# Kernel optimization log

Measured on AMD Instinct MI355X. Metric: run time of the kernel, lower is better.

## Reference

```python
import jax, jax.numpy as jnp
import numpy as np

N, V, D, F, E, H = 10000, 4, 3, 128, 320000, 128
EDGE_IN = 2 * F + 2 * V  # node_features[senders] + node_features[receivers] + lengths_x^2 + lengths_y^2
NORM_CONST = 1.0


def setup_inputs() -> dict:
    key = jax.random.key(0)
    ks = jax.random.split(key, 20)
    w = lambda k, shape: jax.random.normal(k, shape, jnp.float32) * 0.05
    z = lambda n: jnp.zeros((n,), jnp.float32)
    return dict(
        node_positions=jax.random.normal(ks[0], (N, V, D), jnp.float32),
        node_vectors=jax.random.normal(ks[1], (N, V, D), jnp.float32),
        node_features=jax.random.normal(ks[2], (N, F), jnp.float32),
        senders=jax.random.randint(ks[3], (E,), 0, N),
        receivers=jax.random.randint(ks[4], (E,), 0, N),
        We0=w(ks[5], (EDGE_IN, H)), be0=z(H), We1=w(ks[6], (H, H)), be1=z(H),
        Winf=w(ks[7], (H, 1)), binf=z(1),
        Wx0=w(ks[8], (H, H)), bx0=z(H), Wx1=w(ks[9], (H, H)), bx1=z(H), Wxf=w(ks[10], (H, V)),
        Wy0=w(ks[11], (H, H)), by0=z(H), Wy1=w(ks[12], (H, H)), by1=z(H), Wyf=w(ks[13], (H, V)),
        Wh0=w(ks[14], (H + F, H)), bh0=z(H), Wh1=w(ks[15], (H, H)), bh1=z(H), Wh2=w(ks[16], (H, F)), bh2=z(F),
    )


def reference(node_positions, node_vectors, node_features, senders, receivers,
              We0, be0, We1, be1, Winf, binf,
              Wx0, bx0, Wx1, bx1, Wxf,
              Wy0, by0, Wy1, by1, Wyf,
              Wh0, bh0, Wh1, bh1, Wh2, bh2):
    act = jax.nn.silu
    n_nodes = node_positions.shape[0]
    avg = int(np.sqrt(receivers.shape[0]))  # avg_num_neighbours as in source

    def radial(coord):  # coord: [N, V, D]
        d = coord[receivers] - coord[senders]              # [E, V, D]
        l = jnp.sqrt(jnp.sum(d * d, axis=-1) + 1e-8)       # [E, V] safe_norm
        d = d / (NORM_CONST + l[:, :, None])               # normalize=True
        return l, d

    lx, dx = radial(node_positions)
    ly, dy = radial(node_vectors)

    ef = jnp.concatenate([node_features[senders], node_features[receivers],
                          lx ** 2, ly ** 2], axis=-1)      # [E, 264]
    m = act(act(ef @ We0 + be0) @ We1 + be1)               # phi_e, activate_final=True

    # phi_x: torso MLP + no-bias head, tanh
    px = jnp.tanh(act(act(m @ Wx0 + bx0) @ Wx1 + bx1) @ Wxf)          # [E, V]
    shifts_x = jax.ops.segment_sum(dx * px[:, :, None], receivers, num_segments=n_nodes) / avg

    # phi_y: torso MLP + no-bias head, tanh
    py = jnp.tanh(act(act(m @ Wy0 + by0) @ Wy1 + by1) @ Wyf)          # [E, V]
    shifts_y = jax.ops.segment_sum(dy * py[:, :, None], receivers, num_segments=n_nodes) / avg

    # attention gate on messages
    m = m * jax.nn.sigmoid(m @ Winf + binf)
    m_i = jax.ops.segment_sum(m, receivers, num_segments=n_nodes) / avg

    # phi_h (activate_final=False) + residual_h
    hin = jnp.concatenate([m_i, node_features], axis=-1)
    features_out = act(act(hin @ Wh0 + bh0) @ Wh1 + bh1) @ Wh2 + bh2 + node_features

    skip = shifts_y
    vectors_out = skip + node_vectors            # residual_y
    positions_out = shifts_x + node_positions    # x_update='x', residual_x
    return positions_out, vectors_out, features_out, skip
```

## Files before the change

kernel.cpp:

```cpp
#include <hip/hip_runtime.h>
#include <math.h>

#define NN 10000
#define EE 320000
#define TE 32
#define TN 16
#define INV_AVG (1.0f / 565.0f)

#define OUT_POS 0
#define OUT_VEC 120000
#define OUT_FEAT 240000
#define OUT_SKIP 1520000
#define OUT_TOTAL 1640000

#define WS_WE0 0
#define WS_WE1 36864
#define WS_WX0 53248
#define WS_WX1 69632
#define WS_WY0 86016
#define WS_WY1 102400
#define WS_WH0 118784
#define WS_WH1 151552
#define WS_WH2 167936
#define WS_WXF 184320
#define WS_WYF 186368
#define WS_OFF_NF 376832
#define WS_OFF_SORT 2936832
#define WS_OFF_CNT  4216832
#define WS_OFF_CUR  4256832

typedef __attribute__((ext_vector_type(8))) short bfrag;
typedef __attribute__((ext_vector_type(4))) float f4acc;

__device__ __forceinline__ float siluf(float x) {
    return x * __builtin_amdgcn_rcpf(1.0f + __expf(-x));
}
__device__ __forceinline__ float tanh_fast(float x) {
    return 1.0f - 2.0f * __builtin_amdgcn_rcpf(__expf(2.0f * x) + 1.0f);
}
__device__ __forceinline__ float sigmoid_fast(float x) {
    return __builtin_amdgcn_rcpf(1.0f + __expf(-x));
}
__device__ __forceinline__ unsigned int cvt_pk_bf16(float lo, float hi) {
    unsigned int r;
    asm("v_cvt_pk_bf16_f32 %0, %1, %2" : "=v"(r) : "v"(lo), "v"(hi));
    return r;
}
__device__ __forceinline__ unsigned short f2bf(float x) {
    union { float f; unsigned int u; } c; c.f = x;
    unsigned int r = c.u + 0x7FFFu + ((c.u >> 16) & 1u);
    return (unsigned short)(r >> 16);
}
__device__ __forceinline__ float bf2f(unsigned short h) {
    union { unsigned int u; float f; } c; c.u = ((unsigned int)h) << 16; return c.f;
}

__global__ __launch_bounds__(256) void init_kernel(const float* __restrict__ pos,
                                                   float* __restrict__ out,
                                                   int* __restrict__ cnt)
{
    int idx = blockIdx.x * 256 + threadIdx.x;
    if (idx < OUT_TOTAL) out[idx] = (idx < 120000) ? pos[idx] : 0.0f;
    if (idx < NN) cnt[idx] = 0;
}

__global__ __launch_bounds__(256) void prep_all(
    const float* __restrict__ nf, unsigned short* __restrict__ nfb,
    const int* __restrict__ rcv, int* __restrict__ cnt,
    const float* __restrict__ We0, const float* __restrict__ be0,
    const float* __restrict__ We1,
    const float* __restrict__ Wx0, const float* __restrict__ Wx1,
    const float* __restrict__ Wy0, const float* __restrict__ Wy1,
    const float* __restrict__ Wh0, const float* __restrict__ Wh1,
    const float* __restrict__ Wh2,
    const float* __restrict__ Wxf, const float* __restrict__ Wyf,
    unsigned short* __restrict__ wsW)
{
    int tid = blockIdx.x * 256 + threadIdx.x;
    int i = tid * 8;
    if (i < NN * 128) {
        float4 a = *(const float4*)(nf + i);
        float4 b = *(const float4*)(nf + i + 4);
        uint4 pk;
        pk.x = cvt_pk_bf16(a.x, a.y);
        pk.y = cvt_pk_bf16(a.z, a.w);
        pk.z = cvt_pk_bf16(b.x, b.y);
        pk.w = cvt_pk_bf16(b.z, b.w);
        *(uint4*)(nfb + i) = pk;
    }
    int e = tid * 2;
    if (e < EE) {
        atomicAdd(cnt + rcv[e], 1);
        atomicAdd(cnt + rcv[e + 1], 1);
    }
    if (tid >= 23552) return;
    if (tid >= 23040) {
        const float* Wf = (tid < 23296) ? Wxf : Wyf;
        unsigned short* dst = wsW + ((tid < 23296) ? WS_WXF : WS_WYF);
        int rel = tid - ((tid < 23296) ? 23040 : 23296);
        int kc = rel >> 6, lane = rel & 63;
        int lhi = lane >> 4, llo = lane & 15;
        unsigned short* o = dst + ((kc * 64 + lane) << 3);
#pragma unroll
        for (int j = 0; j < 8; ++j) {
            int k = kc * 32 + lhi * 8 + j;
            o[j] = (llo < 4) ? f2bf(Wf[k * 4 + llo]) : (unsigned short)0;
        }
        return;
    }
    const float* W; unsigned short* dst; int Kact = 128, rel; int isWe0 = 0;
    if (tid < 4608)        { W = We0; dst = wsW + WS_WE0; Kact = 264; rel = tid; isWe0 = 1; }
    else if (tid < 14848)  {
        int r = tid - 4608; int m = r >> 11; rel = r & 2047;
        switch (m) {
            case 0: W = We1; dst = wsW + WS_WE1; break;
            case 1: W = Wx0; dst = wsW + WS_WX0; break;
            case 2: W = Wx1; dst = wsW + WS_WX1; break;
            case 3: W = Wy0; dst = wsW + WS_WY0; break;
            default: W = Wy1; dst = wsW + WS_WY1; break;
        }
    }
    else if (tid < 18944)  { W = Wh0; dst = wsW + WS_WH0; Kact = 256; rel = tid - 14848; }
    else if (tid < 20992)  { W = Wh1; dst = wsW + WS_WH1; rel = tid - 18944; }
    else                   { W = Wh2; dst = wsW + WS_WH2; rel = tid - 20992; }
    int lane = rel & 63, oc = (rel >> 6) & 7, kc = rel >> 9;
    int k0 = kc * 32 + ((lane >> 4) << 3);
    int col = oc * 16 + (lane & 15);
    unsigned short* o = dst + (((kc * 8 + oc) * 64 + lane) << 3);
#pragma unroll
    for (int j = 0; j < 8; ++j) {
        int k = k0 + j;
        unsigned short v = 0;
        if (k < Kact) v = f2bf(W[k * 128 + col]);
        else if (isWe0 && k == 264) v = f2bf(be0[col]);
        o[j] = v;
    }
}

__global__ __launch_bounds__(1024) void scan_kernel(const int* __restrict__ cnt,
                                                    int* __restrict__ cursor)
{
    __shared__ int wsum[16];
    int t = threadIdx.x;
    int lane = t & 63, wid = t >> 6;
    int base = t * 10;
    int c[10];
    int s = 0;
#pragma unroll
    for (int i = 0; i < 10; ++i) {
        int b = base + i;
        c[i] = (b < NN) ? cnt[b] : 0;
        s += c[i];
    }
    int run = s;
#pragma unroll
    for (int off = 1; off < 64; off <<= 1) {
        int v = __shfl_up(run, off);
        if (lane >= off) run += v;
    }
    if (lane == 63) wsum[wid] = run;
    __syncthreads();
    if (t < 16) {
        int v = wsum[t];
#pragma unroll
        for (int off = 1; off < 16; off <<= 1) {
            int u = __shfl_up(v, off);
            if (t >= off) v += u;
        }
        wsum[t] = v;
    }
    __syncthreads();
    int wave_excl = (wid == 0) ? 0 : wsum[wid - 1];
    int excl = wave_excl + run - s;
#pragma unroll
    for (int i = 0; i < 10; ++i) {
        int b = base + i;
        if (b < NN) { cursor[b] = excl; excl += c[i]; }
    }
}

__global__ __launch_bounds__(256) void scatter_sort_kernel(const int* __restrict__ rcv,
                                                           int* __restrict__ cursor,
                                                           int* __restrict__ sortedIdx)
{
    int e = blockIdx.x * 256 + threadIdx.x;
    if (e < EE) {
        int slot = atomicAdd(cursor + rcv[e], 1);
        sortedIdx[slot] = e;
    }
}

template<int KC, int MT, int NT>
__device__ __forceinline__ void gemm_lds(const unsigned short* __restrict__ fragW,
                                         const unsigned short* Bld, const int bstride,
                                         const int tile0, const int lane,
                                         f4acc acc[MT][NT])
{
    const int lhi = lane >> 4, llo = lane & 15;
#pragma unroll
    for (int kc = 0; kc < KC; ++kc) {
        bfrag b[NT];
#pragma unroll
        for (int nt = 0; nt < NT; ++nt)
            b[nt] = *(const bfrag*)(Bld + (nt * 16 + llo) * bstride + kc * 32 + lhi * 8);
#pragma unroll
        for (int i = 0; i < MT; ++i) {
            bfrag a = *(const bfrag*)(fragW + (((kc * 8 + tile0 + i) * 64 + lane) << 3));
#pragma unroll
            for (int nt = 0; nt < NT; ++nt)
                acc[i][nt] = __builtin_amdgcn_mfma_f32_16x16x32_bf16(a, b[nt], acc[i][nt], 0, 0, 0);
        }
    }
}

template<int NT>
__device__ __forceinline__ void epilogue_silu_t(f4acc acc[2][NT], const float* __restrict__ bias,
                                                unsigned short* Dld, int lane, int w)
{
    const int lhi = lane >> 4, llo = lane & 15;
#pragma unroll
    for (int i = 0; i < 2; ++i) {
        int ch = (w * 2 + i) * 16 + lhi * 4;
        float4 bv = *(const float4*)(bias + ch);
#pragma unroll
        for (int nt = 0; nt < NT; ++nt) {
            uint2 pk;
            pk.x = cvt_pk_bf16(siluf(acc[i][nt][0] + bv.x), siluf(acc[i][nt][1] + bv.y));
            pk.y = cvt_pk_bf16(siluf(acc[i][nt][2] + bv.z), siluf(acc[i][nt][3] + bv.w));
            *(uint2*)(Dld + (nt * 16 + llo) * 136 + ch) = pk;
        }
    }
}

__device__ __forceinline__ void epilogue_silu_nobias(f4acc acc[2][2],
                                                     unsigned short* Dld, int lane, int w)
{
    const int lhi = lane >> 4, llo = lane & 15;
#pragma unroll
    for (int i = 0; i < 2; ++i) {
        int ch = (w * 2 + i) * 16 + lhi * 4;
#pragma unroll
        for (int nt = 0; nt < 2; ++nt) {
            uint2 pk;
            pk.x = cvt_pk_bf16(siluf(acc[i][nt][0]), siluf(acc[i][nt][1]));
            pk.y = cvt_pk_bf16(siluf(acc[i][nt][2]), siluf(acc[i][nt][3]));
            *(uint2*)(Dld + (nt * 16 + llo) * 136 + ch) = pk;
        }
    }
}

__global__ __launch_bounds__(256, 6) void edge_kernel(
    const float* __restrict__ pos, const float* __restrict__ vec,
    const unsigned short* __restrict__ nfb,
    const int* __restrict__ snd, const int* __restrict__ rcv,
    const int* __restrict__ sortedIdx,
    const unsigned short* __restrict__ wsW,
    const float* __restrict__ be1,
    const float* __restrict__ Winf, const float* __restrict__ binf,
    const float* __restrict__ bx0, const float* __restrict__ bx1,
    const float* __restrict__ by0, const float* __restrict__ by1,
    float* outPos, float* outSkip, float* outFeat)
{
    __shared__ unsigned short L2T[TE * 40];
    __shared__ unsigned short H0[TE * 136];
    __shared__ unsigned short Hm[TE * 136];
    __shared__ float dstore[TE * 24];
    __shared__ float pxy[TE * 8];
    __shared__ float gateacc[TE];
    __shared__ int sidx[TE], ridx[TE];

    const int t = threadIdx.x;
    const int lane = t & 63, w = t >> 6;
    const int lhi = lane >> 4, llo = lane & 15;
    const int e_base = blockIdx.x * TE;

    if (t < TE) {
        int eid = sortedIdx[e_base + t];
        int sn = snd[eid], rn = rcv[eid];
        sidx[t] = sn; ridx[t] = rn;
#pragma unroll
        for (int tensor = 0; tensor < 2; ++tensor) {
            const float* c = tensor ? vec : pos;
#pragma unroll
            for (int v = 0; v < 4; ++v) {
                float d0 = c[rn * 12 + v * 3 + 0] - c[sn * 12 + v * 3 + 0];
                float d1 = c[rn * 12 + v * 3 + 1] - c[sn * 12 + v * 3 + 1];
                float d2 = c[rn * 12 + v * 3 + 2] - c[sn * 12 + v * 3 + 2];
                float ss = fmaf(d0, d0, fmaf(d1, d1, d2 * d2)) + 1e-8f;
                float l = sqrtf(ss);
                float inv = __builtin_amdgcn_rcpf(1.0f + l);
                L2T[t * 40 + tensor * 4 + v] = f2bf(ss);
                dstore[t * 24 + tensor * 12 + v * 3 + 0] = d0 * inv;
                dstore[t * 24 + tensor * 12 + v * 3 + 1] = d1 * inv;
                dstore[t * 24 + tensor * 12 + v * 3 + 2] = d2 * inv;
            }
        }
#pragma unroll
        for (int j = 0; j < 6; ++j)
            *(uint2*)(L2T + t * 40 + 8 + j * 4) = make_uint2(0u, 0u);
        L2T[t * 40 + 8] = 0x3F80u;
    }
    if (t >= 64 && t < 96) gateacc[t - 64] = 0.0f;
    __syncthreads();

    {
        const int sn0 = sidx[llo], sn1 = sidx[16 + llo];
        const int rn0 = ridx[llo], rn1 = ridx[16 + llo];
        const unsigned short* s0 = nfb + sn0 * 128 + lhi * 8;
        const unsigned short* s1 = nfb + sn1 * 128 + lhi * 8;
        const unsigned short* r0 = nfb + rn0 * 128 + lhi * 8;
        const unsigned short* r1 = nfb + rn1 * 128 + lhi * 8;
        const int mt0 = w * 2;
        f4acc acc[2][2];
#pragma unroll
        for (int i = 0; i < 2; ++i) { acc[i][0] = (f4acc){0.f,0.f,0.f,0.f}; acc[i][1] = (f4acc){0.f,0.f,0.f,0.f}; }
#pragma unroll
        for (int kc = 0; kc < 8; ++kc) {
            bfrag b0 = *(const bfrag*)((kc < 4 ? s0 : r0) + (kc & 3) * 32);
            bfrag b1 = *(const bfrag*)((kc < 4 ? s1 : r1) + (kc & 3) * 32);
#pragma unroll
            for (int i = 0; i < 2; ++i) {
                bfrag a = *(const bfrag*)(wsW + WS_WE0 + (((kc * 8 + mt0 + i) * 64 + lane) << 3));
                acc[i][0] = __builtin_amdgcn_mfma_f32_16x16x32_bf16(a, b0, acc[i][0], 0, 0, 0);
                acc[i][1] = __builtin_amdgcn_mfma_f32_16x16x32_bf16(a, b1, acc[i][1], 0, 0, 0);
            }
        }
        {
            bfrag b0 = *(const bfrag*)(L2T + llo * 40 + lhi * 8);
            bfrag b1 = *(const bfrag*)(L2T + (16 + llo) * 40 + lhi * 8);
#pragma unroll
            for (int i = 0; i < 2; ++i) {
                bfrag a = *(const bfrag*)(wsW + WS_WE0 + (((8 * 8 + mt0 + i) * 64 + lane) << 3));
                acc[i][0] = __builtin_amdgcn_mfma_f32_16x16x32_bf16(a, b0, acc[i][0], 0, 0, 0);
                acc[i][1] = __builtin_amdgcn_mfma_f32_16x16x32_bf16(a, b1, acc[i][1], 0, 0, 0);
            }
        }
        epilogue_silu_nobias(acc, H0, lane, w);
    }
    __syncthreads();

    {
        f4acc acc[2][2];
#pragma unroll
        for (int i = 0; i < 2; ++i) { acc[i][0] = (f4acc){0.f,0.f,0.f,0.f}; acc[i][1] = (f4acc){0.f,0.f,0.f,0.f}; }
        gemm_lds<4, 2, 2>(wsW + WS_WE1, H0, 136, w * 2, lane, acc);
        float gp0 = 0.0f, gp1 = 0.0f;
#pragma unroll
        for (int i = 0; i < 2; ++i) {
            int ch = (w * 2 + i) * 16 + lhi * 4;
            float4 bv = *(const float4*)(be1 + ch);
            float4 wg = *(const float4*)(Winf + ch);
#pragma unroll
            for (int nt = 0; nt < 2; ++nt) {
                float v0 = siluf(acc[i][nt][0] + bv.x);
                float v1 = siluf(acc[i][nt][1] + bv.y);
                float v2 = siluf(acc[i][nt][2] + bv.z);
                float v3 = siluf(acc[i][nt][3] + bv.w);
                uint2 pk;
                pk.x = cvt_pk_bf16(v0, v1);
                pk.y = cvt_pk_bf16(v2, v3);
                *(uint2*)(Hm + (nt * 16 + llo) * 136 + ch) = pk;
                float g = fmaf(v0, wg.x, fmaf(v1, wg.y, fmaf(v2, wg.z, v3 * wg.w)));
                if (nt == 0) gp0 += g; else gp1 += g;
            }
        }
        gp0 += __shfl_xor(gp0, 16); gp0 += __shfl_xor(gp0, 32);
        gp1 += __shfl_xor(gp1, 16); gp1 += __shfl_xor(gp1, 32);
        if (lane < 16) {
            atomicAdd(&gateacc[lane], gp0);
            atomicAdd(&gateacc[16 + lane], gp1);
        }
    }
    __syncthreads();

#pragma unroll 1
    for (int br = 0; br < 2; ++br) {
        {
            const unsigned short* fw = wsW + (br ? WS_WY0 : WS_WX0);
            const float* bias = br ? by0 : bx0;
            f4acc acc[2][2];
#pragma unroll
            for (int i = 0; i < 2; ++i) { acc[i][0] = (f4acc){0.f,0.f,0.f,0.f}; acc[i][1] = (f4acc){0.f,0.f,0.f,0.f}; }
            gemm_lds<4, 2, 2>(fw, Hm, 136, w * 2, lane, acc);
            epilogue_silu_t<2>(acc, bias, H0, lane, w);
        }
        __syncthreads();
        {
            const unsigned short* fw = wsW + (br ? WS_WY1 : WS_WX1);
            const float* bias = br ? by1 : bx1;
            f4acc acc[2][2];
#pragma unroll
            for (int i = 0; i < 2; ++i) { acc[i][0] = (f4acc){0.f,0.f,0.f,0.f}; acc[i][1] = (f4acc){0.f,0.f,0.f,0.f}; }
            gemm_lds<4, 2, 2>(fw, H0, 136, w * 2, lane, acc);
            __syncthreads();
            epilogue_silu_t<2>(acc, bias, H0, lane, w);
        }
        __syncthreads();
        if (w < 2) {
            const unsigned short* fw = wsW + (br ? WS_WYF : WS_WXF);
            f4acc h = (f4acc){0.f, 0.f, 0.f, 0.f};
#pragma unroll
            for (int kc = 0; kc < 4; ++kc) {
                bfrag b = *(const bfrag*)(H0 + (w * 16 + llo) * 136 + kc * 32 + lhi * 8);
                bfrag a = *(const bfrag*)(fw + ((kc * 64 + lane) << 3));
                h = __builtin_amdgcn_mfma_f32_16x16x32_bf16(a, b, h, 0, 0, 0);
            }
            if (lhi == 0) {
#pragma unroll
                for (int v = 0; v < 4; ++v)
                    pxy[(w * 16 + llo) * 8 + br * 4 + v] = h[v];
            }
        }
        __syncthreads();
    }

    pxy[t] = tanh_fast(pxy[t]) * INV_AVG;
    if (t < TE) gateacc[t] = sigmoid_fast(gateacc[t] + binf[0]) * INV_AVG;
    __syncthreads();

    if (t < 128) {
        int half = t >> 6, pair = t & 63;
        int jj = pair * 2;
        int e0h = half * 16;
        float a0 = 0.0f, a1 = 0.0f;
        int prev_r = ridx[e0h];
#pragma unroll
        for (int i = 0; i < 16; ++i) {
            int e = e0h + i;
            int r = ridx[e];
            if (r != prev_r) {
                atomicAdd(outFeat + prev_r * 128 + jj, a0);
                atomicAdd(outFeat + prev_r * 128 + jj + 1, a1);
                a0 = a1 = 0.0f;
                prev_r = r;
            }
            unsigned int pk = *(const unsigned int*)(Hm + e * 136 + jj);
            float g = gateacc[e];
            a0 = fmaf(bf2f((unsigned short)(pk & 0xffffu)), g, a0);
            a1 = fmaf(bf2f((unsigned short)(pk >> 16)), g, a1);
        }
        atomicAdd(outFeat + prev_r * 128 + jj, a0);
        atomicAdd(outFeat + prev_r * 128 + jj + 1, a1);
    } else if (t >= 208) {
        int s = t - 208;
        int c = s >> 1, half = s & 1;
        int tensor = (c >= 12) ? 1 : 0;
        int rem = c - tensor * 12;
        int v = rem / 3;
        float* dstp = tensor ? outSkip : outPos;
        int e0h = half * 16;
        float acc = 0.0f;
        int prev_r = ridx[e0h];
#pragma unroll
        for (int i = 0; i < 16; ++i) {
            int e = e0h + i;
            int r = ridx[e];
            if (r != prev_r) {
                atomicAdd(dstp + prev_r * 12 + rem, acc);
                acc = 0.0f;
                prev_r = r;
            }
            acc = fmaf(dstore[e * 24 + c], pxy[e * 8 + tensor * 4 + v], acc);
        }
        atomicAdd(dstp + prev_r * 12 + rem, acc);
    }
}

__global__ __launch_bounds__(256) void node_kernel(
    const float* __restrict__ nf, const unsigned short* __restrict__ nfb,
    const float* __restrict__ nvec,
    const unsigned short* __restrict__ wsW,
    const float* __restrict__ bh0, const float* __restrict__ bh1,
    const float* __restrict__ bh2,
    float* outFeat , float* outVec,
    const float* __restrict__ outSkip)
{
    __shared__ unsigned short A[TN * 264];
    __shared__ unsigned short H1[TN * 136];
    __shared__ unsigned short H2b[TN * 136];
    const int t = threadIdx.x;
    const int lane = t & 63, w = t >> 6;
    const int lhi = lane >> 4, llo = lane & 15;
    const int n_base = blockIdx.x * TN;

#pragma unroll
    for (int it = 0; it < 4; ++it) {
        int idx = t + it * 256;
        int row = idx >> 6, q = idx & 63;
        int n = n_base + row;
        float2 v = make_float2(0.f, 0.f);
        if (n < NN) v = *(const float2*)(outFeat + n * 128 + q * 2);
        *(unsigned int*)(A + row * 264 + q * 2) = cvt_pk_bf16(v.x, v.y);
    }
    {
        int row = t >> 4, q = t & 15;
        int n = n_base + row;
        uint4 v = make_uint4(0u, 0u, 0u, 0u);
        if (n < NN) v = *(const uint4*)(nfb + n * 128 + q * 8);
        *(uint4*)(A + row * 264 + 128 + q * 8) = v;
    }
    __syncthreads();
    {
        f4acc acc[2][1];
        acc[0][0] = (f4acc){0.f,0.f,0.f,0.f}; acc[1][0] = (f4acc){0.f,0.f,0.f,0.f};
        gemm_lds<8, 2, 1>(wsW + WS_WH0, A, 264, w * 2, lane, acc);
        epilogue_silu_t<1>(acc, bh0, H1, lane, w);
    }
    __syncthreads();
    {
        f4acc acc[2][1];
        acc[0][0] = (f4acc){0.f,0.f,0.f,0.f}; acc[1][0] = (f4acc){0.f,0.f,0.f,0.f};
        gemm_lds<4, 2, 1>(wsW + WS_WH1, H1, 136, w * 2, lane, acc);
        epilogue_silu_t<1>(acc, bh1, H2b, lane, w);
    }
    __syncthreads();
    {
        f4acc acc[2][1];
        acc[0][0] = (f4acc){0.f,0.f,0.f,0.f}; acc[1][0] = (f4acc){0.f,0.f,0.f,0.f};
        gemm_lds<4, 2, 1>(wsW + WS_WH2, H2b, 136, w * 2, lane, acc);
#pragma unroll
        for (int i = 0; i < 2; ++i) {
            int ch = (w * 2 + i) * 16 + lhi * 4;
            float4 bv = *(const float4*)(bh2 + ch);
            int n = n_base + llo;
            if (n < NN) {
                float4 r = *(const float4*)(nf + n * 128 + ch);
                float4 o;
                o.x = acc[i][0][0] + bv.x + r.x;
                o.y = acc[i][0][1] + bv.y + r.y;
                o.z = acc[i][0][2] + bv.z + r.z;
                o.w = acc[i][0][3] + bv.w + r.w;
                *(float4*)(outFeat + n * 128 + ch) = o;
            }
        }
    }
    if (t < TN * 12) {
        int n = n_base + t / 12;
        if (n < NN) {
            int g = n_base * 12 + t;
            outVec[g] = outSkip[g] + nvec[g];
        }
    }
}

extern "C" void kernel_launch(void* const* d_in, const int* in_sizes, int n_in,
                              void* d_out, int out_size, void* d_ws, size_t ws_size,
                              hipStream_t stream)
{
    (void)in_sizes; (void)n_in; (void)out_size; (void)ws_size;

    const float* pos  = (const float*)d_in[0];
    const float* vecv = (const float*)d_in[1];
    const float* nf   = (const float*)d_in[2];
    const int*   snd  = (const int*)d_in[3];
    const int*   rcv  = (const int*)d_in[4];
    const float* We0  = (const float*)d_in[5];
    const float* be0  = (const float*)d_in[6];
    const float* We1  = (const float*)d_in[7];
    const float* be1  = (const float*)d_in[8];
    const float* Winf = (const float*)d_in[9];
    const float* binf = (const float*)d_in[10];
    const float* Wx0  = (const float*)d_in[11];
    const float* bx0  = (const float*)d_in[12];
    const float* Wx1  = (const float*)d_in[13];
    const float* bx1  = (const float*)d_in[14];
    const float* Wxf  = (const float*)d_in[15];
    const float* Wy0  = (const float*)d_in[16];
    const float* by0  = (const float*)d_in[17];
    const float* Wy1  = (const float*)d_in[18];
    const float* by1  = (const float*)d_in[19];
    const float* Wyf  = (const float*)d_in[20];
    const float* Wh0  = (const float*)d_in[21];
    const float* bh0  = (const float*)d_in[22];
    const float* Wh1  = (const float*)d_in[23];
    const float* bh1  = (const float*)d_in[24];
    const float* Wh2  = (const float*)d_in[25];
    const float* bh2  = (const float*)d_in[26];

    float* out     = (float*)d_out;
    float* outPos  = out + OUT_POS;
    float* outVec  = out + OUT_VEC;
    float* outFeat = out + OUT_FEAT;
    float* outSkip = out + OUT_SKIP;

    char* ws = (char*)d_ws;
    unsigned short* wsW = (unsigned short*)ws;
    unsigned short* nfb = (unsigned short*)(ws + WS_OFF_NF);
    int* sortedIdx      = (int*)(ws + WS_OFF_SORT);
    int* cnt            = (int*)(ws + WS_OFF_CNT);
    int* cursor         = (int*)(ws + WS_OFF_CUR);

    init_kernel<<<(OUT_TOTAL + 255) / 256, 256, 0, stream>>>(pos, out, cnt);

    prep_all<<<(NN * 128 / 8 + 255) / 256, 256, 0, stream>>>(
        nf, nfb, rcv, cnt,
        We0, be0, We1, Wx0, Wx1, Wy0, Wy1, Wh0, Wh1, Wh2, Wxf, Wyf, wsW);

    scan_kernel<<<1, 1024, 0, stream>>>(cnt, cursor);
    scatter_sort_kernel<<<(EE + 255) / 256, 256, 0, stream>>>(rcv, cursor, sortedIdx);

    edge_kernel<<<EE / TE, 256, 0, stream>>>(
        pos, vecv, nfb, snd, rcv, sortedIdx, wsW,
        be1, Winf, binf,
        bx0, bx1, by0, by1,
        outPos, outSkip, outFeat);

    node_kernel<<<(NN + TN - 1) / TN, 256, 0, stream>>>(
        nf, nfb, vecv, wsW, bh0, bh1, bh2,
        outFeat, outVec, outSkip);
}
```

Baseline: 234.3 us.

## Make edge kernel wave-independent with per-wave 16-edge tiles, no block barriers

```diff
diff --git a/kernel.cpp b/kernel.cpp
--- a/kernel.cpp
+++ b/kernel.cpp
@@ -3,7 +3,6 @@
 
 #define NN 10000
 #define EE 320000
-#define TE 32
 #define TN 16
 #define INV_AVG (1.0f / 565.0f)
 
@@ -32,6 +31,8 @@
 typedef __attribute__((ext_vector_type(8))) short bfrag;
 typedef __attribute__((ext_vector_type(4))) float f4acc;
 
+#define FENCE() asm volatile("s_waitcnt lgkmcnt(0)" ::: "memory")
+
 __device__ __forceinline__ float siluf(float x) {
     return x * __builtin_amdgcn_rcpf(1.0f + __expf(-x));
 }
@@ -190,66 +191,44 @@
     }
 }
 
-template<int KC, int MT, int NT>
-__device__ __forceinline__ void gemm_lds(const unsigned short* __restrict__ fragW,
-                                         const unsigned short* Bld, const int bstride,
-                                         const int tile0, const int lane,
-                                         f4acc acc[MT][NT])
+template<int KC>
+__device__ __forceinline__ void gemm_w(const unsigned short* __restrict__ fragW,
+                                       const unsigned short* Bld, int lane,
+                                       f4acc acc[8])
 {
     const int lhi = lane >> 4, llo = lane & 15;
 #pragma unroll
     for (int kc = 0; kc < KC; ++kc) {
-        bfrag b[NT];
-#pragma unroll
-        for (int nt = 0; nt < NT; ++nt)
-            b[nt] = *(const bfrag*)(Bld + (nt * 16 + llo) * bstride + kc * 32 + lhi * 8);
-#pragma unroll
-        for (int i = 0; i < MT; ++i) {
-            bfrag a = *(const bfrag*)(fragW + (((kc * 8 + tile0 + i) * 64 + lane) << 3));
-#pragma unroll
-            for (int nt = 0; nt < NT; ++nt)
-                acc[i][nt] = __builtin_amdgcn_mfma_f32_16x16x32_bf16(a, b[nt], acc[i][nt], 0, 0, 0);
-        }
-    }
-}
-
-template<int NT>
-__device__ __forceinline__ void epilogue_silu_t(f4acc acc[2][NT], const float* __restrict__ bias,
-                                                unsigned short* Dld, int lane, int w)
+        bfrag b = *(const bfrag*)(Bld + llo * 136 + kc * 32 + lhi * 8);
+#pragma unroll
+        for (int mt = 0; mt < 8; ++mt) {
+            bfrag a = *(const bfrag*)(fragW + (((kc * 8 + mt) * 64 + lane) << 3));
+            acc[mt] = __builtin_amdgcn_mfma_f32_16x16x32_bf16(a, b, acc[mt], 0, 0, 0);
+        }
+    }
+}
+
+template<bool HASBIAS>
+__device__ __forceinline__ void epi_w(f4acc acc[8], const float* __restrict__ bias,
+                                      unsigned short* Dld, int lane)
 {
     const int lhi = lane >> 4, llo = lane & 15;
 #pragma unroll
-    for (int i = 0; i < 2; ++i) {
-        int ch = (w * 2 + i) * 16 + lhi * 4;
-        float4 bv = *(const float4*)(bias + ch);
-#pragma unroll
-        for (int nt = 0; nt < NT; ++nt) {
-            uint2 pk;
-            pk.x = cvt_pk_bf16(siluf(acc[i][nt][0] + bv.x), siluf(acc[i][nt][1] + bv.y));
-            pk.y = cvt_pk_bf16(siluf(acc[i][nt][2] + bv.z), siluf(acc[i][nt][3] + bv.w));
-            *(uint2*)(Dld + (nt * 16 + llo) * 136 + ch) = pk;
-        }
-    }
-}
-
-__device__ __forceinline__ void epilogue_silu_nobias(f4acc acc[2][2],
-                                                     unsigned short* Dld, int lane, int w)
-{
-    const int lhi = lane >> 4, llo = lane & 15;
-#pragma unroll
-    for (int i = 0; i < 2; ++i) {
-        int ch = (w * 2 + i) * 16 + lhi * 4;
-#pragma unroll
-        for (int nt = 0; nt < 2; ++nt) {
-            uint2 pk;
-            pk.x = cvt_pk_bf16(siluf(acc[i][nt][0]), siluf(acc[i][nt][1]));
-            pk.y = cvt_pk_bf16(siluf(acc[i][nt][2]), siluf(acc[i][nt][3]));
-            *(uint2*)(Dld + (nt * 16 + llo) * 136 + ch) = pk;
-        }
-    }
-}
-
-__global__ __launch_bounds__(256, 6) void edge_kernel(
+    for (int mt = 0; mt < 8; ++mt) {
+        int ch = mt * 16 + lhi * 4;
+        float bx = 0.f, by = 0.f, bz = 0.f, bw = 0.f;
+        if (HASBIAS) {
+            float4 bv = *(const float4*)(bias + ch);
+            bx = bv.x; by = bv.y; bz = bv.z; bw = bv.w;
+        }
+        uint2 pk;
+        pk.x = cvt_pk_bf16(siluf(acc[mt][0] + bx), siluf(acc[mt][1] + by));
+        pk.y = cvt_pk_bf16(siluf(acc[mt][2] + bz), siluf(acc[mt][3] + bw));
+        *(uint2*)(Dld + llo * 136 + ch) = pk;
+    }
+}
+
+__global__ __launch_bounds__(256, 3) void edge_kernel(
     const float* __restrict__ pos, const float* __restrict__ vec,
     const unsigned short* __restrict__ nfb,
     const int* __restrict__ snd, const int* __restrict__ rcv,
@@ -261,208 +240,234 @@
     const float* __restrict__ by0, const float* __restrict__ by1,
     float* outPos, float* outSkip, float* outFeat)
 {
-    __shared__ unsigned short L2T[TE * 40];
-    __shared__ unsigned short H0[TE * 136];
-    __shared__ unsigned short Hm[TE * 136];
-    __shared__ float dstore[TE * 24];
-    __shared__ float pxy[TE * 8];
-    __shared__ float gateacc[TE];
-    __shared__ int sidx[TE], ridx[TE];
+    __shared__ __align__(16) unsigned short HwS[4][16 * 136];
+    __shared__ __align__(16) unsigned short MwS[4][16 * 136];
+    __shared__ __align__(16) unsigned short L2TS[4][16 * 40];
+    __shared__ float dstoreS[4][16 * 24];
+    __shared__ float pxyS[4][16 * 8];
+    __shared__ float gatevS[4][16];
+    __shared__ int sidxS[4][16], ridxS[4][16];
 
     const int t = threadIdx.x;
     const int lane = t & 63, w = t >> 6;
     const int lhi = lane >> 4, llo = lane & 15;
-    const int e_base = blockIdx.x * TE;
-
-    if (t < TE) {
-        int eid = sortedIdx[e_base + t];
-        int sn = snd[eid], rn = rcv[eid];
-        sidx[t] = sn; ridx[t] = rn;
-#pragma unroll
-        for (int tensor = 0; tensor < 2; ++tensor) {
-            const float* c = tensor ? vec : pos;
-#pragma unroll
-            for (int v = 0; v < 4; ++v) {
-                float d0 = c[rn * 12 + v * 3 + 0] - c[sn * 12 + v * 3 + 0];
-                float d1 = c[rn * 12 + v * 3 + 1] - c[sn * 12 + v * 3 + 1];
-                float d2 = c[rn * 12 + v * 3 + 2] - c[sn * 12 + v * 3 + 2];
-                float ss = fmaf(d0, d0, fmaf(d1, d1, d2 * d2)) + 1e-8f;
-                float l = sqrtf(ss);
-                float inv = __builtin_amdgcn_rcpf(1.0f + l);
-                L2T[t * 40 + tensor * 4 + v] = f2bf(ss);
-                dstore[t * 24 + tensor * 12 + v * 3 + 0] = d0 * inv;
-                dstore[t * 24 + tensor * 12 + v * 3 + 1] = d1 * inv;
-                dstore[t * 24 + tensor * 12 + v * 3 + 2] = d2 * inv;
+
+    unsigned short* Hw = HwS[w];
+    unsigned short* Mw = MwS[w];
+    unsigned short* L2T = L2TS[w];
+    float* dstore = dstoreS[w];
+    float* pxy = pxyS[w];
+    float* gatev = gatevS[w];
+    int* sidx = sidxS[w];
+    int* ridx = ridxS[w];
+
+    const int e_base = blockIdx.x * 64 + w * 16;
+
+    if (lane < 16) {
+        int eid = sortedIdx[e_base + lane];
+        sidx[lane] = snd[eid];
+        ridx[lane] = rcv[eid];
+    }
+    if (lane < 48) {
+        int e = lane / 3, q = lane - (lane / 3) * 3;
+        uint4 z = make_uint4(q == 0 ? 0x3F80u : 0u, 0u, 0u, 0u);
+        *(uint4*)(L2T + e * 40 + 8 + q * 8) = z;
+    }
+    FENCE();
+#pragma unroll
+    for (int it = 0; it < 2; ++it) {
+        int task = lane + it * 64;
+        int e = task >> 3, sub = task & 7;
+        int tensor = sub >> 2, v = sub & 3;
+        const float* c = tensor ? vec : pos;
+        int sn = sidx[e], rn = ridx[e];
+        float d0 = c[rn * 12 + v * 3 + 0] - c[sn * 12 + v * 3 + 0];
+        float d1 = c[rn * 12 + v * 3 + 1] - c[sn * 12 + v * 3 + 1];
+        float d2 = c[rn * 12 + v * 3 + 2] - c[sn * 12 + v * 3 + 2];
+        float ss = fmaf(d0, d0, fmaf(d1, d1, d2 * d2)) + 1e-8f;
+        float l = sqrtf(ss);
+        float inv = __builtin_amdgcn_rcpf(1.0f + l);
+        L2T[e * 40 + tensor * 4 + v] = f2bf(ss);
+        dstore[e * 24 + tensor * 12 + v * 3 + 0] = d0 * inv;
+        dstore[e * 24 + tensor * 12 + v * 3 + 1] = d1 * inv;
+        dstore[e * 24 + tensor * 12 + v * 3 + 2] = d2 * inv;
+    }
+    FENCE();
+
+    f4acc acc[8];
+#pragma unroll
+    for (int mt = 0; mt < 8; ++mt) acc[mt] = (f4acc){0.f, 0.f, 0.f, 0.f};
+    {
+        const unsigned short* s = nfb + sidx[llo] * 128 + lhi * 8;
+        const unsigned short* r = nfb + ridx[llo] * 128 + lhi * 8;
+#pragma unroll
+        for (int kc = 0; kc < 8; ++kc) {
+            bfrag b = *(const bfrag*)((kc < 4 ? s : r) + (kc & 3) * 32);
+#pragma unroll
+            for (int mt = 0; mt < 8; ++mt) {
+                bfrag a = *(const bfrag*)(wsW + WS_WE0 + (((kc * 8 + mt) * 64 + lane) << 3));
+                acc[mt] = __builtin_amdgcn_mfma_f32_16x16x32_bf16(a, b, acc[mt], 0, 0, 0);
             }
         }
-#pragma unroll
-        for (int j = 0; j < 6; ++j)
-            *(uint2*)(L2T + t * 40 + 8 + j * 4) = make_uint2(0u, 0u);
-        L2T[t * 40 + 8] = 0x3F80u;
-    }
-    if (t >= 64 && t < 96) gateacc[t - 64] = 0.0f;
-    __syncthreads();
+        {
+            bfrag b = *(const bfrag*)(L2T + llo * 40 + lhi * 8);
+#pragma unroll
+            for (int mt = 0; mt < 8; ++mt) {
+                bfrag a = *(const bfrag*)(wsW + WS_WE0 + (((64 + mt) * 64 + lane) << 3));
+                acc[mt] = __builtin_amdgcn_mfma_f32_16x16x32_bf16(a, b, acc[mt], 0, 0, 0);
+            }
+        }
+        epi_w<false>(acc, nullptr, Hw, lane);
+    }
+    FENCE();
 
     {
-        const int sn0 = sidx[llo], sn1 = sidx[16 + llo];
-        const int rn0 = ridx[llo], rn1 = ridx[16 + llo];
-        const unsigned short* s0 = nfb + sn0 * 128 + lhi * 8;
-        const unsigned short* s1 = nfb + sn1 * 128 + lhi * 8;
-        const unsigned short* r0 = nfb + rn0 * 128 + lhi * 8;
-        const unsigned short* r1 = nfb + rn1 * 128 + lhi * 8;
-        const int mt0 = w * 2;
-        f4acc acc[2][2];
-#pragma unroll
-        for (int i = 0; i < 2; ++i) { acc[i][0] = (f4acc){0.f,0.f,0.f,0.f}; acc[i][1] = (f4acc){0.f,0.f,0.f,0.f}; }
-#pragma unroll
-        for (int kc = 0; kc < 8; ++kc) {
-            bfrag b0 = *(const bfrag*)((kc < 4 ? s0 : r0) + (kc & 3) * 32);
-            bfrag b1 = *(const bfrag*)((kc < 4 ? s1 : r1) + (kc & 3) * 32);
-#pragma unroll
-            for (int i = 0; i < 2; ++i) {
-                bfrag a = *(const bfrag*)(wsW + WS_WE0 + (((kc * 8 + mt0 + i) * 64 + lane) << 3));
-                acc[i][0] = __builtin_amdgcn_mfma_f32_16x16x32_bf16(a, b0, acc[i][0], 0, 0, 0);
-                acc[i][1] = __builtin_amdgcn_mfma_f32_16x16x32_bf16(a, b1, acc[i][1], 0, 0, 0);
-            }
-        }
-        {
-            bfrag b0 = *(const bfrag*)(L2T + llo * 40 + lhi * 8);
-            bfrag b1 = *(const bfrag*)(L2T + (16 + llo) * 40 + lhi * 8);
-#pragma unroll
-            for (int i = 0; i < 2; ++i) {
-                bfrag a = *(const bfrag*)(wsW + WS_WE0 + (((8 * 8 + mt0 + i) * 64 + lane) << 3));
-                acc[i][0] = __builtin_amdgcn_mfma_f32_16x16x32_bf16(a, b0, acc[i][0], 0, 0, 0);
-                acc[i][1] = __builtin_amdgcn_mfma_f32_16x16x32_bf16(a, b1, acc[i][1], 0, 0, 0);
-            }
-        }
-        epilogue_silu_nobias(acc, H0, lane, w);
-    }
-    __syncthreads();
-
-    {
-        f4acc acc[2][2];
-#pragma unroll
-        for (int i = 0; i < 2; ++i) { acc[i][0] = (f4acc){0.f,0.f,0.f,0.f}; acc[i][1] = (f4acc){0.f,0.f,0.f,0.f}; }
-        gemm_lds<4, 2, 2>(wsW + WS_WE1, H0, 136, w * 2, lane, acc);
-        float gp0 = 0.0f, gp1 = 0.0f;
-#pragma unroll
-        for (int i = 0; i < 2; ++i) {
-            int ch = (w * 2 + i) * 16 + lhi * 4;
+#pragma unroll
+        for (int mt = 0; mt < 8; ++mt) acc[mt] = (f4acc){0.f, 0.f, 0.f, 0.f};
+        gemm_w<4>(wsW + WS_WE1, Hw, lane, acc);
+        float gp = 0.0f;
+#pragma unroll
+        for (int mt = 0; mt < 8; ++mt) {
+            int ch = mt * 16 + lhi * 4;
             float4 bv = *(const float4*)(be1 + ch);
             float4 wg = *(const float4*)(Winf + ch);
-#pragma unroll
-            for (int nt = 0; nt < 2; ++nt) {
-                float v0 = siluf(acc[i][nt][0] + bv.x);
-                float v1 = siluf(acc[i][nt][1] + bv.y);
-                float v2 = siluf(acc[i][nt][2] + bv.z);
-                float v3 = siluf(acc[i][nt][3] + bv.w);
-                uint2 pk;
-                pk.x = cvt_pk_bf16(v0, v1);
-                pk.y = cvt_pk_bf16(v2, v3);
-                *(uint2*)(Hm + (nt * 16 + llo) * 136 + ch) = pk;
-                float g = fmaf(v0, wg.x, fmaf(v1, wg.y, fmaf(v2, wg.z, v3 * wg.w)));
-                if (nt == 0) gp0 += g; else gp1 += g;
-            }
-        }
-        gp0 += __shfl_xor(gp0, 16); gp0 += __shfl_xor(gp0, 32);
-        gp1 += __shfl_xor(gp1, 16); gp1 += __shfl_xor(gp1, 32);
-        if (lane < 16) {
-            atomicAdd(&gateacc[lane], gp0);
-            atomicAdd(&gateacc[16 + lane], gp1);
-        }
-    }
-    __syncthreads();
+            float v0 = siluf(acc[mt][0] + bv.x);
+            float v1 = siluf(acc[mt][1] + bv.y);
+            float v2 = siluf(acc[mt][2] + bv.z);
+            float v3 = siluf(acc[mt][3] + bv.w);
+            uint2 pk;
+            pk.x = cvt_pk_bf16(v0, v1);
+            pk.y = cvt_pk_bf16(v2, v3);
+            *(uint2*)(Mw + llo * 136 + ch) = pk;
+            gp += fmaf(v0, wg.x, fmaf(v1, wg.y, fmaf(v2, wg.z, v3 * wg.w)));
+        }
+        gp += __shfl_xor(gp, 16);
+        gp += __shfl_xor(gp, 32);
+        if (lhi == 0) gatev[llo] = sigmoid_fast(gp + binf[0]) * INV_AVG;
+    }
+    FENCE();
 
 #pragma unroll 1
     for (int br = 0; br < 2; ++br) {
         {
-            const unsigned short* fw = wsW + (br ? WS_WY0 : WS_WX0);
-            const float* bias = br ? by0 : bx0;
-            f4acc acc[2][2];
-#pragma unroll
-            for (int i = 0; i < 2; ++i) { acc[i][0] = (f4acc){0.f,0.f,0.f,0.f}; acc[i][1] = (f4acc){0.f,0.f,0.f,0.f}; }
-            gemm_lds<4, 2, 2>(fw, Hm, 136, w * 2, lane, acc);
-            epilogue_silu_t<2>(acc, bias, H0, lane, w);
-        }
-        __syncthreads();
+#pragma unroll
+            for (int mt = 0; mt < 8; ++mt) acc[mt] = (f4acc){0.f, 0.f, 0.f, 0.f};
+            gemm_w<4>(wsW + (br ? WS_WY0 : WS_WX0), Mw, lane, acc);
+            epi_w<true>(acc, br ? by0 : bx0, Hw, lane);
+        }
+        FENCE();
         {
-            const unsigned short* fw = wsW + (br ? WS_WY1 : WS_WX1);
-            const float* bias = br ? by1 : bx1;
-            f4acc acc[2][2];
-#pragma unroll
-            for (int i = 0; i < 2; ++i) { acc[i][0] = (f4acc){0.f,0.f,0.f,0.f}; acc[i][1] = (f4acc){0.f,0.f,0.f,0.f}; }
-            gemm_lds<4, 2, 2>(fw, H0, 136, w * 2, lane, acc);
-            __syncthreads();
-            epilogue_silu_t<2>(acc, bias, H0, lane, w);
-        }
-        __syncthreads();
-        if (w < 2) {
+#pragma unroll
+            for (int mt = 0; mt < 8; ++mt) acc[mt] = (f4acc){0.f, 0.f, 0.f, 0.f};
+            gemm_w<4>(wsW + (br ? WS_WY1 : WS_WX1), Hw, lane, acc);
+            FENCE();
+            epi_w<true>(acc, br ? by1 : bx1, Hw, lane);
+        }
+        FENCE();
+        {
+            f4acc h = (f4acc){0.f, 0.f, 0.f, 0.f};
             const unsigned short* fw = wsW + (br ? WS_WYF : WS_WXF);
-            f4acc h = (f4acc){0.f, 0.f, 0.f, 0.f};
 #pragma unroll
             for (int kc = 0; kc < 4; ++kc) {
-                bfrag b = *(const bfrag*)(H0 + (w * 16 + llo) * 136 + kc * 32 + lhi * 8);
+                bfrag b = *(const bfrag*)(Hw + llo * 136 + kc * 32 + lhi * 8);
                 bfrag a = *(const bfrag*)(fw + ((kc * 64 + lane) << 3));
                 h = __builtin_amdgcn_mfma_f32_16x16x32_bf16(a, b, h, 0, 0, 0);
             }
             if (lhi == 0) {
 #pragma unroll
                 for (int v = 0; v < 4; ++v)
-                    pxy[(w * 16 + llo) * 8 + br * 4 + v] = h[v];
+                    pxy[llo * 8 + br * 4 + v] = h[v];
             }
         }
-        __syncthreads();
-    }
-
-    pxy[t] = tanh_fast(pxy[t]) * INV_AVG;
-    if (t < TE) gateacc[t] = sigmoid_fast(gateacc[t] + binf[0]) * INV_AVG;
-    __syncthreads();
-
-    if (t < 128) {
-        int half = t >> 6, pair = t & 63;
-        int jj = pair * 2;
-        int e0h = half * 16;
+        FENCE();
+    }
+
+    pxy[lane] = tanh_fast(pxy[lane]) * INV_AVG;
+    pxy[lane + 64] = tanh_fast(pxy[lane + 64]) * INV_AVG;
+    FENCE();
+
+    {
+        int jj = lane * 2;
         float a0 = 0.0f, a1 = 0.0f;
-        int prev_r = ridx[e0h];
+        int prev_r = ridx[0];
 #pragma unroll
         for (int i = 0; i < 16; ++i) {
-            int e = e0h + i;
-            int r = ridx[e];
+            int r = ridx[i];
             if (r != prev_r) {
                 atomicAdd(outFeat + prev_r * 128 + jj, a0);
                 atomicAdd(outFeat + prev_r * 128 + jj + 1, a1);
                 a0 = a1 = 0.0f;
                 prev_r = r;
             }
-            unsigned int pk = *(const unsigned int*)(Hm + e * 136 + jj);
-            float g = gateacc[e];
+            unsigned int pk = *(const unsigned int*)(Mw + i * 136 + jj);
+            float g = gatev[i];
             a0 = fmaf(bf2f((unsigned short)(pk & 0xffffu)), g, a0);
             a1 = fmaf(bf2f((unsigned short)(pk >> 16)), g, a1);
         }
         atomicAdd(outFeat + prev_r * 128 + jj, a0);
         atomicAdd(outFeat + prev_r * 128 + jj + 1, a1);
-    } else if (t >= 208) {
-        int s = t - 208;
-        int c = s >> 1, half = s & 1;
+    }
+    if (lane < 24) {
+        int c = lane;
         int tensor = (c >= 12) ? 1 : 0;
         int rem = c - tensor * 12;
         int v = rem / 3;
         float* dstp = tensor ? outSkip : outPos;
-        int e0h = half * 16;
-        float acc = 0.0f;
-        int prev_r = ridx[e0h];
+        float accv = 0.0f;
+        int prev_r = ridx[0];
 #pragma unroll
         for (int i = 0; i < 16; ++i) {
-            int e = e0h + i;
-            int r = ridx[e];
+            int r = ridx[i];
             if (r != prev_r) {
-                atomicAdd(dstp + prev_r * 12 + rem, acc);
-                acc = 0.0f;
+                atomicAdd(dstp + prev_r * 12 + rem, accv);
+                accv = 0.0f;
                 prev_r = r;
             }
-            acc = fmaf(dstore[e * 24 + c], pxy[e * 8 + tensor * 4 + v], acc);
-        }
-        atomicAdd(dstp + prev_r * 12 + rem, acc);
+            accv = fmaf(dstore[i * 24 + c], pxy[i * 8 + tensor * 4 + v], accv);
+        }
+        atomicAdd(dstp + prev_r * 12 + rem, accv);
+    }
+}
+
+template<int KC, int MT, int NT>
+__device__ __forceinline__ void gemm_lds(const unsigned short* __restrict__ fragW,
+                                         const unsigned short* Bld, const int bstride,
+                                         const int tile0, const int lane,
+                                         f4acc acc[MT][NT])
+{
+    const int lhi = lane >> 4, llo = lane & 15;
+#pragma unroll
+    for (int kc = 0; kc < KC; ++kc) {
+        bfrag b[NT];
+#pragma unroll
+        for (int nt = 0; nt < NT; ++nt)
+            b[nt] = *(const bfrag*)(Bld + (nt * 16 + llo) * bstride + kc * 32 + lhi * 8);
+#pragma unroll
+        for (int i = 0; i < MT; ++i) {
+            bfrag a = *(const bfrag*)(fragW + (((kc * 8 + tile0 + i) * 64 + lane) << 3));
+#pragma unroll
+            for (int nt = 0; nt < NT; ++nt)
+                acc[i][nt] = __builtin_amdgcn_mfma_f32_16x16x32_bf16(a, b[nt], acc[i][nt], 0, 0, 0);
+        }
+    }
+}
+
+template<int NT>
+__device__ __forceinline__ void epilogue_silu_t(f4acc acc[2][NT], const float* __restrict__ bias,
+                                                unsigned short* Dld, int lane, int w)
+{
+    const int lhi = lane >> 4, llo = lane & 15;
+#pragma unroll
+    for (int i = 0; i < 2; ++i) {
+        int ch = (w * 2 + i) * 16 + lhi * 4;
+        float4 bv = *(const float4*)(bias + ch);
+#pragma unroll
+        for (int nt = 0; nt < NT; ++nt) {
+            uint2 pk;
+            pk.x = cvt_pk_bf16(siluf(acc[i][nt][0] + bv.x), siluf(acc[i][nt][1] + bv.y));
+            pk.y = cvt_pk_bf16(siluf(acc[i][nt][2] + bv.z), siluf(acc[i][nt][3] + bv.w));
+            *(uint2*)(Dld + (nt * 16 + llo) * 136 + ch) = pk;
+        }
     }
 }
 
@@ -599,7 +604,7 @@
     scan_kernel<<<1, 1024, 0, stream>>>(cnt, cursor);
     scatter_sort_kernel<<<(EE + 255) / 256, 256, 0, stream>>>(rcv, cursor, sortedIdx);
 
-    edge_kernel<<<EE / TE, 256, 0, stream>>>(
+    edge_kernel<<<EE / 64, 256, 0, stream>>>(
         pos, vecv, nfb, snd, rcv, sortedIdx, wsW,
         be1, Winf, binf,
         bx0, bx1, by0, by1,
```

After: 285.2 us. 1.22x slower.
